# Kernel optimization log

Measured on AMD Instinct MI355X. Metric: run time of the kernel, lower is better.

## Reference

```python
import jax, jax.numpy as jnp
import numpy as np

N = 100000
E = 600000
IN_DIM = 256
H0 = 128
H1 = 64
EPS = 1e-5


def setup_inputs() -> dict:
    key = jax.random.key(0)
    ks = jax.random.split(key, 12)
    x = jax.random.normal(ks[0], (N, IN_DIM), dtype=jnp.float32)
    edge_index = jax.random.randint(ks[1], (2, E), 0, N, dtype=jnp.int64)
    edge_weight = jax.random.uniform(ks[2], (E,), dtype=jnp.float32)
    def lin(k, fan_in, fan_out):
        bound = 1.0 / np.sqrt(fan_in)
        k1, k2 = jax.random.split(k)
        W = jax.random.uniform(k1, (fan_in, fan_out), minval=-bound, maxval=bound, dtype=jnp.float32)
        b = jax.random.uniform(k2, (fan_out,), minval=-bound, maxval=bound, dtype=jnp.float32)
        return W, b
    W0, b0 = lin(ks[3], IN_DIM, H0)
    W1, b1 = lin(ks[4], H0, H0)
    W2, b2 = lin(ks[5], H0, H0)
    pW, pb = lin(ks[6], H0, H1)
    return {
        'x': x, 'edge_index': edge_index, 'edge_weight': edge_weight,
        'bn_gamma': jnp.ones((IN_DIM,), jnp.float32), 'bn_beta': jnp.zeros((IN_DIM,), jnp.float32),
        'W0': W0, 'b0': b0, 'W1': W1, 'b1': b1, 'W2': W2, 'b2': b2,
        'pbn_gamma': jnp.ones((H0,), jnp.float32), 'pbn_beta': jnp.zeros((H0,), jnp.float32),
        'pW': pW, 'pb': pb,
    }


def batchnorm(x, gamma, beta):
    # BatchNorm1d training-mode forward: per-feature batch statistics over nodes
    mean = jnp.mean(x, axis=0)
    var = jnp.mean(jnp.square(x - mean), axis=0)  # biased var, as torch BN forward
    return (x - mean) * jax.lax.rsqrt(var + EPS) * gamma + beta


def gcn_conv(x, src, dst, norm, W, b):
    # PyG GCNConv (add_self_loops=False): transform then normalized aggregation
    h = x @ W                                   # [N, out]
    msg = norm[:, None] * h[src]                # gather + scale, [E, out]
    out = jax.ops.segment_sum(msg, dst, num_segments=N)  # scatter-add
    return out + b


def reference(x, edge_index, edge_weight, bn_gamma, bn_beta, W0, b0, W1, b1, W2, b2, pbn_gamma, pbn_beta, pW, pb):
    src, dst = edge_index[0], edge_index[1]
    # gcn_norm without self loops: D^-1/2 A D^-1/2
    deg = jax.ops.segment_sum(edge_weight, dst, num_segments=N)
    dis = jnp.where(deg > 0, jax.lax.rsqrt(jnp.maximum(deg, EPS)), 0.0)
    norm = dis[src] * edge_weight * dis[dst]    # [E]

    h = batchnorm(x, bn_gamma, bn_beta)
    h = jax.nn.relu(gcn_conv(h, src, dst, norm, W0, b0))
    h = jax.nn.relu(gcn_conv(h, src, dst, norm, W1, b1))
    h = jax.nn.relu(gcn_conv(h, src, dst, norm, W2, b2))
    # project head: BN -> Linear -> ReLU
    h = batchnorm(h, pbn_gamma, pbn_beta)
    h = jax.nn.relu(h @ pW + pb)
    return h
```

## Files before the change

kernel.cpp:

```cpp
#include <hip/hip_runtime.h>


constexpr int NN    = 100000;
constexpr int NEDGE = 600000;
constexpr int INDIM = 256;
constexpr int HD    = 128;
constexpr int OUTD  = 64;
constexpr int EB    = (NEDGE + 255) / 256;
constexpr int SB    = 1024;
constexpr int NB    = (NN + 255) / 256;
constexpr int WB    = 257;
constexpr int GG    = (NN + 127) / 128;
constexpr int A2B   = 1024;
#define EPSV 1e-5f

typedef __bf16 bf16x8 __attribute__((ext_vector_type(8)));
typedef float  f32x4  __attribute__((ext_vector_type(4)));

__device__ __forceinline__ float bf2f(unsigned short u) {
    unsigned int v = ((unsigned int)u) << 16;
    return __builtin_bit_cast(float, v);
}
__device__ __forceinline__ unsigned short f2bf(float f) {
    __bf16 h = (__bf16)f;
    return __builtin_bit_cast(unsigned short, h);
}
__device__ __forceinline__ void atomAdd(float* p, float v) {
    unsafeAtomicAdd(p, v);
}

template <int K, int M, bool RELU_OUT, bool OUT_BF16>
__device__ __forceinline__ void mgemm_body(int bid, int tid, char* smem,
                                           const unsigned short* __restrict__ A,
                                           const unsigned short* __restrict__ Bt,
                                           const float* __restrict__ outBias,
                                           void* __restrict__ Craw, int n) {
    constexpr int BK  = 64;
    constexpr int LDA = BK + 8;
    unsigned short* As = (unsigned short*)smem;
    unsigned short* Bs = As + 128 * LDA;

    const int wave = tid >> 6, lane = tid & 63;
    const int quad = lane >> 4, mrow = lane & 15;
    const int row0 = bid * 128;

    constexpr int RT = (M == 128) ? 4 : 2;
    constexpr int CT = 4;
    const int rowbase = (M == 128) ? ((wave >> 1) * 64) : (wave * 32);
    const int colbase = (M == 128) ? ((wave & 1) * 64) : 0;

    f32x4 acc[RT][CT];
#pragma unroll
    for (int i = 0; i < RT; i++)
#pragma unroll
        for (int j = 0; j < CT; j++) acc[i][j] = (f32x4){0.f, 0.f, 0.f, 0.f};

    for (int k0 = 0; k0 < K; k0 += BK) {
        if (k0) __syncthreads();
#pragma unroll
        for (int p = 0; p < 4; p++) {
            int c   = p * 256 + tid;
            int r   = c >> 3;
            int c8  = (c & 7) * 8;
            int grow = row0 + r;
            uint4 u = make_uint4(0, 0, 0, 0);
            if (grow < n) u = *(const uint4*)&A[(size_t)grow * K + k0 + c8];
            *(uint4*)&As[r * LDA + c8] = u;
        }
#pragma unroll
        for (int p = 0; p < M / 32; p++) {
            int c  = p * 256 + tid;
            int r  = c >> 3;
            int c8 = (c & 7) * 8;
            *(uint4*)&Bs[r * LDA + c8] = *(const uint4*)&Bt[(size_t)r * K + k0 + c8];
        }
        __syncthreads();

#pragma unroll
        for (int ks = 0; ks < BK; ks += 32) {
            bf16x8 af[RT], bfr[CT];
#pragma unroll
            for (int i = 0; i < RT; i++)
                af[i] = *(const bf16x8*)&As[(rowbase + i * 16 + mrow) * LDA + ks + quad * 8];
#pragma unroll
            for (int j = 0; j < CT; j++)
                bfr[j] = *(const bf16x8*)&Bs[(colbase + j * 16 + mrow) * LDA + ks + quad * 8];
#pragma unroll
            for (int i = 0; i < RT; i++)
#pragma unroll
                for (int j = 0; j < CT; j++)
                    acc[i][j] = __builtin_amdgcn_mfma_f32_16x16x32_bf16(
                        af[i], bfr[j], acc[i][j], 0, 0, 0);
        }
    }

#pragma unroll
    for (int i = 0; i < RT; i++) {
#pragma unroll
        for (int r = 0; r < 4; r++) {
            int row = row0 + rowbase + i * 16 + quad * 4 + r;
            if (row < n) {
#pragma unroll
                for (int j = 0; j < CT; j++) {
                    int col = colbase + j * 16 + mrow;
                    float v = acc[i][j][r];
                    if (outBias) v += outBias[col];
                    if (RELU_OUT) v = fmaxf(v, 0.f);
                    if (OUT_BF16)
                        ((unsigned short*)Craw)[(size_t)row * M + col] = f2bf(v);
                    else
                        ((float*)Craw)[(size_t)row * M + col] = v;
                }
            }
        }
    }
}

__device__ __forceinline__ void gather8(const unsigned short* __restrict__ tg,
                                        const uint2* __restrict__ edata,
                                        int i, int beg, int end, float* acc) {
    uint4 v[8]; float w[8];
#pragma unroll
    for (int k = 0; k < 8; k++) {
        int  idx = i + k;
        bool ok  = idx < end;
        uint2 ed = edata[ok ? idx : beg];
        w[k] = ok ? __builtin_bit_cast(float, ed.y) : 0.f;
        v[k] = *(const uint4*)&tg[(size_t)ed.x * HD];
    }
#pragma unroll
    for (int k = 0; k < 8; k++) {
        acc[0] += w[k] * bf2f((unsigned short)(v[k].x & 0xffff));
        acc[1] += w[k] * bf2f((unsigned short)(v[k].x >> 16));
        acc[2] += w[k] * bf2f((unsigned short)(v[k].y & 0xffff));
        acc[3] += w[k] * bf2f((unsigned short)(v[k].y >> 16));
        acc[4] += w[k] * bf2f((unsigned short)(v[k].z & 0xffff));
        acc[5] += w[k] * bf2f((unsigned short)(v[k].z >> 16));
        acc[6] += w[k] * bf2f((unsigned short)(v[k].w & 0xffff));
        acc[7] += w[k] * bf2f((unsigned short)(v[k].w >> 16));
    }
}

__global__ __launch_bounds__(256) void fagg_gemm_k(const unsigned short* __restrict__ t,
                                                   const int* __restrict__ rowptr,
                                                   const uint2* __restrict__ edata,
                                                   const float* __restrict__ bias,
                                                   const unsigned short* __restrict__ Bt,
                                                   unsigned short* __restrict__ Cout,
                                                   int n) {
    constexpr int LDAa = HD + 8;
    constexpr int LDAb = 64 + 8;
    __shared__ unsigned short As[128 * LDAa];
    __shared__ unsigned short Bs[HD * LDAb];

    const int tid  = threadIdx.x;
    const int row0 = blockIdx.x * 128;

    {
        const int g  = tid >> 4;
        const int gl = tid & 15;
        const unsigned short* tg = t + gl * 8;
        float4 bb0 = *(const float4*)&bias[gl * 8];
        float4 bb1 = *(const float4*)&bias[gl * 8 + 4];
        for (int rr = 0; rr < 8; rr++) {
            int node = row0 + g * 8 + rr;
            float acc[8];
#pragma unroll
            for (int j = 0; j < 8; j++) acc[j] = 0.f;
            if (node < n) {
                int beg = rowptr[node], end = rowptr[node + 1];
                for (int i = beg; i < end; i += 8)
                    gather8(tg, edata, i, beg, end, acc);
            }
            float r0 = fmaxf(acc[0] + bb0.x, 0.f), r1 = fmaxf(acc[1] + bb0.y, 0.f);
            float r2 = fmaxf(acc[2] + bb0.z, 0.f), r3 = fmaxf(acc[3] + bb0.w, 0.f);
            float r4 = fmaxf(acc[4] + bb1.x, 0.f), r5 = fmaxf(acc[5] + bb1.y, 0.f);
            float r6 = fmaxf(acc[6] + bb1.z, 0.f), r7 = fmaxf(acc[7] + bb1.w, 0.f);
            uint4 o;
            o.x = (unsigned int)f2bf(r0) | ((unsigned int)f2bf(r1) << 16);
            o.y = (unsigned int)f2bf(r2) | ((unsigned int)f2bf(r3) << 16);
            o.z = (unsigned int)f2bf(r4) | ((unsigned int)f2bf(r5) << 16);
            o.w = (unsigned int)f2bf(r6) | ((unsigned int)f2bf(r7) << 16);
            *(uint4*)&As[(g * 8 + rr) * LDAa + gl * 8] = o;
        }
    }

    const int wave = tid >> 6, lane = tid & 63;
    const int quad = lane >> 4, mrow = lane & 15;
    const int rowbase = (wave >> 1) * 64;
    const int colbase = (wave & 1) * 64;

    f32x4 acc[4][4];
#pragma unroll
    for (int i = 0; i < 4; i++)
#pragma unroll
        for (int j = 0; j < 4; j++) acc[i][j] = (f32x4){0.f, 0.f, 0.f, 0.f};

    for (int k0 = 0; k0 < HD; k0 += 64) {
        if (k0) __syncthreads();
#pragma unroll
        for (int p = 0; p < 4; p++) {
            int c  = p * 256 + tid;
            int r  = c >> 3;
            int c8 = (c & 7) * 8;
            *(uint4*)&Bs[r * LDAb + c8] = *(const uint4*)&Bt[(size_t)r * HD + k0 + c8];
        }
        __syncthreads();
#pragma unroll
        for (int ks = 0; ks < 64; ks += 32) {
            bf16x8 af[4], bfr[4];
#pragma unroll
            for (int i = 0; i < 4; i++)
                af[i] = *(const bf16x8*)&As[(rowbase + i * 16 + mrow) * LDAa + k0 + ks + quad * 8];
#pragma unroll
            for (int j = 0; j < 4; j++)
                bfr[j] = *(const bf16x8*)&Bs[(colbase + j * 16 + mrow) * LDAb + ks + quad * 8];
#pragma unroll
            for (int i = 0; i < 4; i++)
#pragma unroll
                for (int j = 0; j < 4; j++)
                    acc[i][j] = __builtin_amdgcn_mfma_f32_16x16x32_bf16(
                        af[i], bfr[j], acc[i][j], 0, 0, 0);
        }
    }

#pragma unroll
    for (int i = 0; i < 4; i++) {
#pragma unroll
        for (int r = 0; r < 4; r++) {
            int row = row0 + rowbase + i * 16 + quad * 4 + r;
            if (row < n) {
#pragma unroll
                for (int j = 0; j < 4; j++) {
                    int col = colbase + j * 16 + mrow;
                    Cout[(size_t)row * HD + col] = f2bf(acc[i][j][r]);
                }
            }
        }
    }
}

__global__ __launch_bounds__(256) void front_k(const int* __restrict__ dst,
                                               const float* __restrict__ ew,
                                               float* __restrict__ deg,
                                               int* __restrict__ cnt,
                                               const float* __restrict__ x,
                                               float* __restrict__ sums,
                                               unsigned short* __restrict__ xb) {
    __shared__ float red[256 * 8];
    const int tid = threadIdx.x;
    if (blockIdx.x < EB) {
        int i = blockIdx.x * 256 + tid;
        if (i < NEDGE) {
            int d = dst[i];
            atomAdd(&deg[d], ew[i]);
            atomicAdd(&cnt[d], 1);
        }
        return;
    }
    const int bid = blockIdx.x - EB;
    const int cg  = tid & 63;
    const int rs  = tid >> 6;
    float s0 = 0.f, s1 = 0.f, s2 = 0.f, s3 = 0.f;
    float q0 = 0.f, q1 = 0.f, q2 = 0.f, q3 = 0.f;
    for (int r0 = bid * 16; r0 < NN; r0 += SB * 16) {
        float4 v[4];
#pragma unroll
        for (int j = 0; j < 4; j++)
            v[j] = *(const float4*)&x[(size_t)(r0 + rs + j * 4) * INDIM + cg * 4];
#pragma unroll
        for (int j = 0; j < 4; j++) {
            s0 += v[j].x; s1 += v[j].y; s2 += v[j].z; s3 += v[j].w;
            q0 += v[j].x * v[j].x; q1 += v[j].y * v[j].y;
            q2 += v[j].z * v[j].z; q3 += v[j].w * v[j].w;
            unsigned int w0 = (unsigned int)f2bf(v[j].x) | ((unsigned int)f2bf(v[j].y) << 16);
            unsigned int w1 = (unsigned int)f2bf(v[j].z) | ((unsigned int)f2bf(v[j].w) << 16);
            *(uint2*)&xb[(size_t)(r0 + rs + j * 4) * INDIM + cg * 4] = make_uint2(w0, w1);
        }
    }
    red[tid * 8 + 0] = s0; red[tid * 8 + 1] = s1;
    red[tid * 8 + 2] = s2; red[tid * 8 + 3] = s3;
    red[tid * 8 + 4] = q0; red[tid * 8 + 5] = q1;
    red[tid * 8 + 6] = q2; red[tid * 8 + 7] = q3;
    __syncthreads();
    int cgr = tid >> 2, j = tid & 3;
    float a = 0.f, b = 0.f;
#pragma unroll
    for (int r2 = 0; r2 < 4; r2++) {
        a += red[(r2 * 64 + cgr) * 8 + j];
        b += red[(r2 * 64 + cgr) * 8 + 4 + j];
    }
    atomAdd(&sums[tid], a);
    atomAdd(&sums[INDIM + tid], b);
}

__global__ __launch_bounds__(256) void mid_k(const int* __restrict__ cnt,
                                             int* __restrict__ rowptr,
                                             int* __restrict__ bsum,
                                             const float* __restrict__ stats,
                                             const float* __restrict__ gamma,
                                             const float* __restrict__ beta,
                                             const float* __restrict__ W0,
                                             const float* __restrict__ W1,
                                             const float* __restrict__ W2,
                                             unsigned short* __restrict__ W0t,
                                             unsigned short* __restrict__ W1t,
                                             unsigned short* __restrict__ W2t,
                                             float* __restrict__ d0, float invN) {
    __shared__ float sm[512];
    const int tid = threadIdx.x;
    if (blockIdx.x < NB) {
        int* s = (int*)sm;
        int i = blockIdx.x * 256 + tid;
        s[tid] = (i < NN) ? cnt[i] : 0;
        __syncthreads();
        for (int d = 1; d < 256; d <<= 1) {
            int t = (tid >= d) ? s[tid - d] : 0;
            __syncthreads();
            s[tid] += t;
            __syncthreads();
        }
        if (i < NN) rowptr[i + 1] = s[tid];
        if (tid == 255) bsum[blockIdx.x] = s[255];
        return;
    }
    const int b = blockIdx.x - NB;
    float* sA = sm;
    float* sC = sm + 256;
    {
        float mean = stats[tid] * invN;
        float var  = stats[INDIM + tid] * invN - mean * mean;
        float a    = gamma[tid] * rsqrtf(var + EPSV);
        sA[tid] = a;
        sC[tid] = beta[tid] - mean * a;
    }
    __syncthreads();
    if (b < 128) {
        int i = b * 256 + tid, k = i >> 7, j = i & 127;
        W0t[(size_t)j * INDIM + k] = f2bf(W0[i] * sA[k]);
    } else if (b < 192) {
        int i = (b - 128) * 256 + tid, k = i >> 7, j = i & 127;
        W1t[(size_t)j * HD + k] = f2bf(W1[i]);
    } else if (b < 256) {
        int i = (b - 192) * 256 + tid, k = i >> 7, j = i & 127;
        W2t[(size_t)j * HD + k] = f2bf(W2[i]);
    } else {
        if (tid < HD) {
            float s = 0.f;
            for (int ff = 0; ff < INDIM; ff++) s += sC[ff] * W0[ff * HD + tid];
            d0[tid] = s;
        }
    }
}

__global__ __launch_bounds__(512) void scan2_k(int* __restrict__ bsum, int nb) {
    __shared__ int s[512];
    s[threadIdx.x] = (threadIdx.x < (unsigned)nb) ? bsum[threadIdx.x] : 0;
    __syncthreads();
    for (int d = 1; d < 512; d <<= 1) {
        int t = (threadIdx.x >= d) ? s[threadIdx.x - d] : 0;
        __syncthreads();
        s[threadIdx.x] += t;
        __syncthreads();
    }
    if (threadIdx.x < (unsigned)nb) bsum[threadIdx.x] = s[threadIdx.x];
}

__global__ __launch_bounds__(256) void scan3_k(int* __restrict__ rowptr,
                                               const int* __restrict__ bsum,
                                               int* __restrict__ cursor, int n) {
    int i = blockIdx.x * 256 + threadIdx.x;
    if (i == 0) { rowptr[0] = 0; cursor[0] = 0; }
    if (i < n) {
        int v = rowptr[i + 1];
        if (blockIdx.x > 0) v += bsum[blockIdx.x - 1];
        rowptr[i + 1] = v;
        if (i + 1 < n) cursor[i + 1] = v;
    }
}

__global__ __launch_bounds__(256) void sg0_k(const int* __restrict__ src,
                                             const int* __restrict__ dst,
                                             const float* __restrict__ ew,
                                             const float* __restrict__ deg,
                                             int* __restrict__ cursor,
                                             uint2* __restrict__ edata,
                                             const unsigned short* __restrict__ xb,
                                             const unsigned short* __restrict__ W0t,
                                             const float* __restrict__ d0,
                                             unsigned short* __restrict__ tbufA) {
    __shared__ char smem[(128 * 72 + 128 * 72) * 2];
    if (blockIdx.x < EB) {
        int i = blockIdx.x * 256 + threadIdx.x;
        if (i < NEDGE) {
            int s = src[i], d = dst[i];
            float ds = deg[s], dd = deg[d];
            float is = ds > 0.f ? rsqrtf(fmaxf(ds, EPSV)) : 0.f;
            float id = dd > 0.f ? rsqrtf(fmaxf(dd, EPSV)) : 0.f;
            float nm = is * ew[i] * id;
            int p = atomicAdd(&cursor[d], 1);
            edata[p] = make_uint2((unsigned)s, __builtin_bit_cast(unsigned, nm));
        }
        return;
    }
    mgemm_body<INDIM, HD, false, true>(blockIdx.x - EB, threadIdx.x, smem,
                                       xb, W0t, d0, tbufA, NN);
}

__global__ __launch_bounds__(256) void agg2_stats_k(const unsigned short* __restrict__ t,
                                                    const int* __restrict__ rowptr,
                                                    const uint2* __restrict__ edata,
                                                    const float* __restrict__ bias,
                                                    unsigned short* __restrict__ agg,
                                                    float* __restrict__ sums, int n) {
    const int tid = threadIdx.x, g = tid >> 4, gl = tid & 15;
    const unsigned short* tg = t + gl * 8;
    float4 bb0 = *(const float4*)&bias[gl * 8];
    float4 bb1 = *(const float4*)&bias[gl * 8 + 4];
    float ssum[8], ssq[8];
#pragma unroll
    for (int j = 0; j < 8; j++) { ssum[j] = 0.f; ssq[j] = 0.f; }

    for (int node0 = blockIdx.x * 16; node0 < n; node0 += A2B * 16) {
        int node = node0 + g;
        float acc[8];
#pragma unroll
        for (int j = 0; j < 8; j++) acc[j] = 0.f;
        if (node < n) {
            int beg = rowptr[node], end = rowptr[node + 1];
            for (int i = beg; i < end; i += 8)
                gather8(tg, edata, i, beg, end, acc);
        }
        float r[8];
        r[0] = fmaxf(acc[0] + bb0.x, 0.f); r[1] = fmaxf(acc[1] + bb0.y, 0.f);
        r[2] = fmaxf(acc[2] + bb0.z, 0.f); r[3] = fmaxf(acc[3] + bb0.w, 0.f);
        r[4] = fmaxf(acc[4] + bb1.x, 0.f); r[5] = fmaxf(acc[5] + bb1.y, 0.f);
        r[6] = fmaxf(acc[6] + bb1.z, 0.f); r[7] = fmaxf(acc[7] + bb1.w, 0.f);
        if (node < n) {
            uint4 o;
            o.x = (unsigned int)f2bf(r[0]) | ((unsigned int)f2bf(r[1]) << 16);
            o.y = (unsigned int)f2bf(r[2]) | ((unsigned int)f2bf(r[3]) << 16);
            o.z = (unsigned int)f2bf(r[4]) | ((unsigned int)f2bf(r[5]) << 16);
            o.w = (unsigned int)f2bf(r[6]) | ((unsigned int)f2bf(r[7]) << 16);
            *(uint4*)&agg[(size_t)node * HD + gl * 8] = o;
#pragma unroll
            for (int j = 0; j < 8; j++) { ssum[j] += r[j]; ssq[j] += r[j] * r[j]; }
        }
    }

    __shared__ float red[256 * 16];
#pragma unroll
    for (int j = 0; j < 8; j++) {
        red[tid * 16 + j]     = ssum[j];
        red[tid * 16 + 8 + j] = ssq[j];
    }
    __syncthreads();
    if (tid < HD) {
        int glr = tid >> 3, j = tid & 7;
        float a = 0.f, b = 0.f;
#pragma unroll
        for (int g2 = 0; g2 < 16; g2++) {
            a += red[(g2 * 16 + glr) * 16 + j];
            b += red[(g2 * 16 + glr) * 16 + 8 + j];
        }
        atomAdd(&sums[tid], a);
        atomAdd(&sums[HD + tid], b);
    }
}

__global__ __launch_bounds__(256) void wprep2_k(const float* __restrict__ stats2,
                                                const float* __restrict__ gamma,
                                                const float* __restrict__ beta,
                                                const float* __restrict__ pW,
                                                const float* __restrict__ pb,
                                                unsigned short* __restrict__ pWt,
                                                float* __restrict__ dfin, float invN) {
    __shared__ float sA[HD], sC[HD];
    int f = threadIdx.x;
    if (f < HD) {
        float mean = stats2[f] * invN;
        float var  = stats2[HD + f] * invN - mean * mean;
        float a    = gamma[f] * rsqrtf(var + EPSV);
        sA[f] = a;
        sC[f] = beta[f] - mean * a;
    }
    __syncthreads();
    int b = blockIdx.x, tid = threadIdx.x;
    if (b < 32) {
        int i = b * 256 + tid, k = i >> 6, j = i & 63;
        pWt[(size_t)j * HD + k] = f2bf(pW[i] * sA[k]);
    } else {
        if (tid < OUTD) {
            float s = pb[tid];
            for (int ff = 0; ff < HD; ff++) s += sC[ff] * pW[ff * OUTD + tid];
            dfin[tid] = s;
        }
    }
}

__global__ __launch_bounds__(256) void gemm3_k(const unsigned short* __restrict__ A,
                                               const unsigned short* __restrict__ Bt,
                                               const float* __restrict__ outBias,
                                               float* __restrict__ C, int n) {
    __shared__ char smem[(128 * 72 + OUTD * 72) * 2];
    mgemm_body<HD, OUTD, true, false>(blockIdx.x, threadIdx.x, smem,
                                      A, Bt, outBias, C, n);
}

extern "C" void kernel_launch(void* const* d_in, const int* in_sizes, int n_in,
                              void* d_out, int out_size, void* d_ws, size_t ws_size,
                              hipStream_t stream) {
    const float* x        = (const float*)d_in[0];
    const int*   ei       = (const int*)d_in[1];
    const float* ew       = (const float*)d_in[2];
    const float* bn_gamma = (const float*)d_in[3];
    const float* bn_beta  = (const float*)d_in[4];
    const float* W0       = (const float*)d_in[5];
    const float* b0       = (const float*)d_in[6];
    const float* W1       = (const float*)d_in[7];
    const float* b1       = (const float*)d_in[8];
    const float* W2       = (const float*)d_in[9];
    const float* b2       = (const float*)d_in[10];
    const float* pgamma   = (const float*)d_in[11];
    const float* pbeta    = (const float*)d_in[12];
    const float* pW       = (const float*)d_in[13];
    const float* pb       = (const float*)d_in[14];
    float* out = (float*)d_out;

    const int* srcp = ei;
    const int* dstp = ei + NEDGE;

    char*  base = (char*)d_ws;
    size_t off  = 0;
    auto carve = [&](size_t bytes) -> void* {
        void* p = (void*)(base + off);
        off = (off + bytes + 255) & ~(size_t)255;
        return p;
    };
    float*          deg    = (float*)carve(NN * 4);
    int*            cnt    = (int*)carve(NN * 4);
    float*          stats  = (float*)carve(2 * INDIM * 4);
    float*          stats2 = (float*)carve(2 * HD * 4);
    int*            rowptr = (int*)carve((NN + 1) * 4);
    int*            cursor = (int*)carve(NN * 4);
    int*            bsum   = (int*)carve(512 * 4);
    uint2*          edata  = (uint2*)carve((size_t)NEDGE * 8);
    float*          d0     = (float*)carve(HD * 4);
    float*          dfin   = (float*)carve(OUTD * 4);
    unsigned short* W0t    = (unsigned short*)carve((size_t)INDIM * HD * 2);
    unsigned short* W1t    = (unsigned short*)carve((size_t)HD * HD * 2);
    unsigned short* W2t    = (unsigned short*)carve((size_t)HD * HD * 2);
    unsigned short* pWt    = (unsigned short*)carve((size_t)HD * OUTD * 2);
    unsigned short* xb     = (unsigned short*)carve((size_t)NN * INDIM * 2);
    unsigned short* tbufA  = (unsigned short*)carve((size_t)NN * HD * 2);
    unsigned short* tbufB  = (unsigned short*)carve((size_t)NN * HD * 2);
    unsigned short* aggb   = (unsigned short*)carve((size_t)NN * HD * 2);
    (void)ws_size;

    hipMemsetAsync(deg, 0, (size_t)((char*)stats2 - (char*)deg) + 2 * HD * 4, stream);

    front_k<<<EB + SB, 256, 0, stream>>>(dstp, ew, deg, cnt, x, stats, xb);

    mid_k<<<NB + WB, 256, 0, stream>>>(cnt, rowptr, bsum, stats, bn_gamma, bn_beta,
                                       W0, W1, W2, W0t, W1t, W2t, d0, 1.f / NN);
    scan2_k<<<1, 512, 0, stream>>>(bsum, NB);
    scan3_k<<<NB, 256, 0, stream>>>(rowptr, bsum, cursor, NN);

    sg0_k<<<EB + GG, 256, 0, stream>>>(srcp, dstp, ew, deg, cursor, edata,
                                       xb, W0t, d0, tbufA);

    fagg_gemm_k<<<GG, 256, 0, stream>>>(tbufA, rowptr, edata, b0, W1t, tbufB, NN);
    fagg_gemm_k<<<GG, 256, 0, stream>>>(tbufB, rowptr, edata, b1, W2t, tbufA, NN);

    agg2_stats_k<<<A2B, 256, 0, stream>>>(tbufA, rowptr, edata, b2, aggb, stats2, NN);

    wprep2_k<<<33, 256, 0, stream>>>(stats2, pgamma, pbeta, pW, pb, pWt, dfin,
                                     1.f / NN);
    gemm3_k<<<GG, 256, 0, stream>>>(aggb, pWt, dfin, out, NN);

    (void)n_in; (void)in_sizes; (void)out_size;
}
```

Baseline: 475.6 us.

## Compute degree norm from CSR and fold edge normalization into first aggregation

```diff
diff --git a/kernel.cpp b/kernel.cpp
--- a/kernel.cpp
+++ b/kernel.cpp
@@ -116,17 +116,32 @@
     }
 }
 
+template <bool L1>
 __device__ __forceinline__ void gather8(const unsigned short* __restrict__ tg,
-                                        const uint2* __restrict__ edata,
+                                        uint2* __restrict__ edata,
+                                        const float* __restrict__ dis,
+                                        float id, int gl,
                                         int i, int beg, int end, float* acc) {
-    uint4 v[8]; float w[8];
+    uint4 v[8]; float w[8]; uint2 ed[8];
 #pragma unroll
     for (int k = 0; k < 8; k++) {
         int  idx = i + k;
         bool ok  = idx < end;
-        uint2 ed = edata[ok ? idx : beg];
-        w[k] = ok ? __builtin_bit_cast(float, ed.y) : 0.f;
-        v[k] = *(const uint4*)&tg[(size_t)ed.x * HD];
+        ed[k] = edata[ok ? idx : beg];
+    }
+#pragma unroll
+    for (int k = 0; k < 8; k++) {
+        bool ok = (i + k) < end;
+        float wt = __builtin_bit_cast(float, ed[k].y);
+        if (L1) wt = dis[ed[k].x] * wt * id;
+        w[k] = ok ? wt : 0.f;
+        v[k] = *(const uint4*)&tg[(size_t)ed[k].x * HD];
+    }
+    if (L1) {
+#pragma unroll
+        for (int k = 0; k < 8; k++)
+            if (gl == 0 && (i + k) < end)
+                edata[i + k].y = __builtin_bit_cast(unsigned, w[k]);
     }
 #pragma unroll
     for (int k = 0; k < 8; k++) {
@@ -141,9 +156,11 @@
     }
 }
 
+template <bool L1>
 __global__ __launch_bounds__(256) void fagg_gemm_k(const unsigned short* __restrict__ t,
                                                    const int* __restrict__ rowptr,
-                                                   const uint2* __restrict__ edata,
+                                                   uint2* __restrict__ edata,
+                                                   const float* __restrict__ dis,
                                                    const float* __restrict__ bias,
                                                    const unsigned short* __restrict__ Bt,
                                                    unsigned short* __restrict__ Cout,
@@ -169,8 +186,9 @@
             for (int j = 0; j < 8; j++) acc[j] = 0.f;
             if (node < n) {
                 int beg = rowptr[node], end = rowptr[node + 1];
+                float id = L1 ? dis[node] : 0.f;
                 for (int i = beg; i < end; i += 8)
-                    gather8(tg, edata, i, beg, end, acc);
+                    gather8<L1>(tg, edata, dis, id, gl, i, beg, end, acc);
             }
             float r0 = fmaxf(acc[0] + bb0.x, 0.f), r1 = fmaxf(acc[1] + bb0.y, 0.f);
             float r2 = fmaxf(acc[2] + bb0.z, 0.f), r3 = fmaxf(acc[3] + bb0.w, 0.f);
@@ -241,9 +259,8 @@
 }
 
 __global__ __launch_bounds__(256) void front_k(const int* __restrict__ dst,
-                                               const float* __restrict__ ew,
-                                               float* __restrict__ deg,
                                                int* __restrict__ cnt,
+                                               int* __restrict__ rank,
                                                const float* __restrict__ x,
                                                float* __restrict__ sums,
                                                unsigned short* __restrict__ xb) {
@@ -253,8 +270,7 @@
         int i = blockIdx.x * 256 + tid;
         if (i < NEDGE) {
             int d = dst[i];
-            atomAdd(&deg[d], ew[i]);
-            atomicAdd(&cnt[d], 1);
+            rank[i] = atomicAdd(&cnt[d], 1);
         }
         return;
     }
@@ -367,23 +383,21 @@
 }
 
 __global__ __launch_bounds__(256) void scan3_k(int* __restrict__ rowptr,
-                                               const int* __restrict__ bsum,
-                                               int* __restrict__ cursor, int n) {
+                                               const int* __restrict__ bsum, int n) {
     int i = blockIdx.x * 256 + threadIdx.x;
-    if (i == 0) { rowptr[0] = 0; cursor[0] = 0; }
+    if (i == 0) rowptr[0] = 0;
     if (i < n) {
         int v = rowptr[i + 1];
         if (blockIdx.x > 0) v += bsum[blockIdx.x - 1];
         rowptr[i + 1] = v;
-        if (i + 1 < n) cursor[i + 1] = v;
     }
 }
 
 __global__ __launch_bounds__(256) void sg0_k(const int* __restrict__ src,
                                              const int* __restrict__ dst,
                                              const float* __restrict__ ew,
-                                             const float* __restrict__ deg,
-                                             int* __restrict__ cursor,
+                                             const int* __restrict__ rank,
+                                             const int* __restrict__ rowptr,
                                              uint2* __restrict__ edata,
                                              const unsigned short* __restrict__ xb,
                                              const unsigned short* __restrict__ W0t,
@@ -394,12 +408,8 @@
         int i = blockIdx.x * 256 + threadIdx.x;
         if (i < NEDGE) {
             int s = src[i], d = dst[i];
-            float ds = deg[s], dd = deg[d];
-            float is = ds > 0.f ? rsqrtf(fmaxf(ds, EPSV)) : 0.f;
-            float id = dd > 0.f ? rsqrtf(fmaxf(dd, EPSV)) : 0.f;
-            float nm = is * ew[i] * id;
-            int p = atomicAdd(&cursor[d], 1);
-            edata[p] = make_uint2((unsigned)s, __builtin_bit_cast(unsigned, nm));
+            int p = rowptr[d] + rank[i];
+            edata[p] = make_uint2((unsigned)s, __builtin_bit_cast(unsigned, ew[i]));
         }
         return;
     }
@@ -407,9 +417,22 @@
                                        xb, W0t, d0, tbufA, NN);
 }
 
+__global__ __launch_bounds__(256) void degnorm_k(const int* __restrict__ rowptr,
+                                                 const uint2* __restrict__ edata,
+                                                 float* __restrict__ dis) {
+    int n = blockIdx.x * 256 + threadIdx.x;
+    if (n < NN) {
+        int beg = rowptr[n], end = rowptr[n + 1];
+        float s = 0.f;
+        for (int j = beg; j < end; j++)
+            s += __builtin_bit_cast(float, edata[j].y);
+        dis[n] = (s > 0.f) ? rsqrtf(fmaxf(s, EPSV)) : 0.f;
+    }
+}
+
 __global__ __launch_bounds__(256) void agg2_stats_k(const unsigned short* __restrict__ t,
                                                     const int* __restrict__ rowptr,
-                                                    const uint2* __restrict__ edata,
+                                                    uint2* __restrict__ edata,
                                                     const float* __restrict__ bias,
                                                     unsigned short* __restrict__ agg,
                                                     float* __restrict__ sums, int n) {
@@ -429,7 +452,7 @@
         if (node < n) {
             int beg = rowptr[node], end = rowptr[node + 1];
             for (int i = beg; i < end; i += 8)
-                gather8(tg, edata, i, beg, end, acc);
+                gather8<false>(tg, edata, nullptr, 0.f, gl, i, beg, end, acc);
         }
         float r[8];
         r[0] = fmaxf(acc[0] + bb0.x, 0.f); r[1] = fmaxf(acc[1] + bb0.y, 0.f);
@@ -537,12 +560,12 @@
         off = (off + bytes + 255) & ~(size_t)255;
         return p;
     };
-    float*          deg    = (float*)carve(NN * 4);
     int*            cnt    = (int*)carve(NN * 4);
     float*          stats  = (float*)carve(2 * INDIM * 4);
     float*          stats2 = (float*)carve(2 * HD * 4);
     int*            rowptr = (int*)carve((NN + 1) * 4);
-    int*            cursor = (int*)carve(NN * 4);
+    int*            rank   = (int*)carve((size_t)NEDGE * 4);
+    float*          dis    = (float*)carve(NN * 4);
     int*            bsum   = (int*)carve(512 * 4);
     uint2*          edata  = (uint2*)carve((size_t)NEDGE * 8);
     float*          d0     = (float*)carve(HD * 4);
@@ -557,20 +580,22 @@
     unsigned short* aggb   = (unsigned short*)carve((size_t)NN * HD * 2);
     (void)ws_size;
 
-    hipMemsetAsync(deg, 0, (size_t)((char*)stats2 - (char*)deg) + 2 * HD * 4, stream);
-
-    front_k<<<EB + SB, 256, 0, stream>>>(dstp, ew, deg, cnt, x, stats, xb);
+    hipMemsetAsync(cnt, 0, (size_t)((char*)stats2 - (char*)cnt) + 2 * HD * 4, stream);
+
+    front_k<<<EB + SB, 256, 0, stream>>>(dstp, cnt, rank, x, stats, xb);
 
     mid_k<<<NB + WB, 256, 0, stream>>>(cnt, rowptr, bsum, stats, bn_gamma, bn_beta,
                                        W0, W1, W2, W0t, W1t, W2t, d0, 1.f / NN);
     scan2_k<<<1, 512, 0, stream>>>(bsum, NB);
-    scan3_k<<<NB, 256, 0, stream>>>(rowptr, bsum, cursor, NN);
-
-    sg0_k<<<EB + GG, 256, 0, stream>>>(srcp, dstp, ew, deg, cursor, edata,
+    scan3_k<<<NB, 256, 0, stream>>>(rowptr, bsum, NN);
+
+    sg0_k<<<EB + GG, 256, 0, stream>>>(srcp, dstp, ew, rank, rowptr, edata,
                                        xb, W0t, d0, tbufA);
 
-    fagg_gemm_k<<<GG, 256, 0, stream>>>(tbufA, rowptr, edata, b0, W1t, tbufB, NN);
-    fagg_gemm_k<<<GG, 256, 0, stream>>>(tbufB, rowptr, edata, b1, W2t, tbufA, NN);
+    degnorm_k<<<NB, 256, 0, stream>>>(rowptr, edata, dis);
+
+    fagg_gemm_k<true><<<GG, 256, 0, stream>>>(tbufA, rowptr, edata, dis, b0, W1t, tbufB, NN);
+    fagg_gemm_k<false><<<GG, 256, 0, stream>>>(tbufB, rowptr, edata, dis, b1, W2t, tbufA, NN);
 
     agg2_stats_k<<<A2B, 256, 0, stream>>>(tbufA, rowptr, edata, b2, aggb, stats2, NN);
 
```

Result: faster. 455.3 us (-4.3%).
